# Optimization experiments

Measured on AMD Instinct MI355X. Metric: run time of the kernel, lower is better.

## Reference

```python
import jax, jax.numpy as jnp
import numpy as np

NC = 1      # constants.nc (Game-of-Life grid channels)
GRID = 32
PAD_ITERS = 31


def _iterated_wrap_idx(n, p):
    # Faithfully simulate p iterations of circular pad-1 on a growing axis.
    # NOTE: this is NOT a single wrap-pad of p; the border alternates 0/n-1.
    idx = np.arange(n)
    for _ in range(p):
        idx = np.concatenate([idx[-1:], idx, idx[:1]])
    return jnp.asarray(idx)

_IDX = _iterated_wrap_idx(GRID, PAD_ITERS)  # length 94, static


def _pad(x):
    # one gather per spatial dim replaces the 31-iteration concat loop
    return x[:, :, _IDX][:, :, :, _IDX]


def _conv(x, w, b, stride):
    y = jax.lax.conv_general_dilated(
        x, w, window_strides=(stride, stride), padding='VALID',
        dimension_numbers=('NCHW', 'OIHW', 'NCHW'))
    return y + b[None, :, None, None]


def setup_inputs() -> dict:
    key = jax.random.key(0)
    ks = jax.random.split(key, 7)
    B = 16
    s_in = 1.0 / np.sqrt(NC * 32 * 32)      # fan-in init, keeps activations sane
    s_hid = 1.0 / np.sqrt(32 * 32 * 32)
    s_out = 1.0 / np.sqrt(32)
    return {
        'x': jax.random.normal(ks[0], (B, NC, GRID, GRID), jnp.float32),
        'in_w': jax.random.normal(ks[1], (32, NC, 32, 32), jnp.float32) * s_in,
        'in_b': jnp.zeros((32,), jnp.float32),
        'convs_w': jax.random.normal(ks[2], (20, 32, 32, 32, 32), jnp.float32) * s_hid,
        'convs_b': jnp.zeros((20, 32), jnp.float32),
        'out_w': jax.random.normal(ks[3], (NC, 32, 1, 1), jnp.float32) * s_out,
        'out_b': jnp.zeros((NC,), jnp.float32),
    }


def reference(x, in_w, in_b, convs_w, convs_b, out_w, out_b):
    # in_conv: pad(31 iters) + conv k=32 s=2 (no ReLU, as in original)
    h = _conv(_pad(x), in_w, in_b, 2)           # [B,32,32,32]

    def step(h, wb):
        w, b = wb
        h = jax.nn.relu(_conv(_pad(h), w, b, 2))
        return h, None

    h, _ = jax.lax.scan(step, h, (convs_w, convs_b))  # 20 hidden layers
    return _conv(h, out_w, out_b, 1)             # 1x1 out conv, no activation
```

## Files before the change

### kernel.cpp

```cpp
#include <hip/hip_runtime.h>


typedef _Float16 f16;
typedef _Float16 f16x8 __attribute__((ext_vector_type(8)));
typedef float f32x4 __attribute__((ext_vector_type(4)));
typedef float f32x16 __attribute__((ext_vector_type(16)));
typedef int i32x4 __attribute__((ext_vector_type(4)));

__device__ __forceinline__ int mwrap(int j) {
  int t = j - 31;
  if ((unsigned)t <= 31u) return t;
  if (t < 0) return (j & 1) ? 0 : 31;
  return (j & 1) ? 0 : 31;
}


#define GLD16(dst, off, base, imm)                                          \
  asm volatile("global_load_dwordx4 %0, %1, %2 offset:%3"                   \
               : "=v"(dst) : "v"(off), "s"(base), "i"(imm) : "memory")

#define PINN(N)                                                             \
  asm volatile("s_waitcnt vmcnt(" #N ")" ::: "memory");                     \
  __builtin_amdgcn_sched_barrier(0)

#define MFMAC(AUSE, FD)                                                      \
  {                                                                          \
    __builtin_amdgcn_s_setprio(1);                                           \
    _Pragma("unroll")                                                        \
    for (int kyi_ = 0; kyi_ < 4; ++kyi_) {                                   \
      _Pragma("unroll")                                                      \
      for (int kxh_ = 0; kxh_ < 2; ++kxh_) {                                 \
        const f16x8 a_ = __builtin_bit_cast(f16x8, AUSE[kyi_ * 2 + kxh_]);   \
        acc0 = __builtin_amdgcn_mfma_f32_32x32x16_f16(a_, FD[kyi_][kxh_],    \
                                                      acc0, 0, 0, 0);        \
        acc1 = __builtin_amdgcn_mfma_f32_32x32x16_f16(a_, FD[kyi_ + 2][kxh_],\
                                                      acc1, 0, 0, 0);        \
      }                                                                      \
    }                                                                        \
    __builtin_amdgcn_s_setprio(0);                                           \
  }

template <int CIN, bool RELU, bool PRE>
__global__ __launch_bounds__(512, 2) void gemm3(
    const void* __restrict__ Wv,
    const f16* __restrict__ hp_in,
    const float* __restrict__ bias,
    f16* __restrict__ hp_out) {
  __shared__ float Red[8][2][1024];
  __shared__ __align__(16) f16 Stage[8][2][576];

  const int tid = threadIdx.x;
  const int lane = tid & 63;
  const int w = tid >> 6;
  const int ox = lane & 31;
  const int s = lane >> 5;

  const int pair0 = blockIdx.x * 2;
  const int b = pair0 >> 5;
  const int oy0 = pair0 & 31;

  const int r0 = lane / 12, g0 = lane - r0 * 12;
  const int y0 = mwrap(2 * oy0 + 4 * w + r0);
  const int y5 = mwrap(2 * oy0 + 4 * w + 5);
  int* SW = (int*)&Stage[w][0][0];
  const int wo0 = r0 * 48 + g0 * 4;
  const int wo1 = 5 * 48 + (4 + lane) * 4;
  const int bi = ox + 4 * s;

  f32x16 acc0 = {}, acc1 = {};
  i32x4 A0[8], A1[8];
  f16x8 F[6][2];
  i32x4 saA = {}, sbA = {}, saB = {}, sbB = {};

  const f16* Wl = (const f16*)Wv;
  const f16* hpb = hp_in + (size_t)b * CIN * 3072;
  const uint32_t aBase = (uint32_t)(w * 8192 + lane * 16);
  const uint32_t s0Base = (uint32_t)(y0 * 192 + g0 * 16);
  const uint32_t s1Base = (uint32_t)(y5 * 192 + 64 + (lane & 7) * 16);

  auto loadAasm = [&](int c, i32x4* dst) {
    const uint32_t o0 = aBase + (uint32_t)c * 65536u;
    const uint32_t o1 = o0 + 4096u;
    GLD16(dst[0], o0, Wl, 0);    GLD16(dst[1], o0, Wl, 1024);
    GLD16(dst[2], o0, Wl, 2048); GLD16(dst[3], o0, Wl, 3072);
    GLD16(dst[4], o1, Wl, 0);    GLD16(dst[5], o1, Wl, 1024);
    GLD16(dst[6], o1, Wl, 2048); GLD16(dst[7], o1, Wl, 3072);
  };
  auto loadSasm = [&](int c, i32x4& a, i32x4& bq) {
    const uint32_t o0 = s0Base + (uint32_t)c * 6144u;
    const uint32_t o1 = s1Base + (uint32_t)c * 6144u;
    GLD16(a, o0, hpb, 0);
    GLD16(bq, o1, hpb, 0);
  };

  auto loadA_c = [&](int c, i32x4* dst) {
#pragma unroll
    for (int kyi = 0; kyi < 4; ++kyi) {
#pragma unroll
      for (int kxh = 0; kxh < 2; ++kxh) {
        const int ky = 4 * w + kyi;
        const int chunk = (c * 32 + ky) * 2 + kxh;
        if constexpr (PRE) {
          dst[kyi * 2 + kxh] = *(const i32x4*)(Wl + (size_t)chunk * 512 + lane * 8);
        } else {
          const float* Wf = (const float*)Wv;
          const float* sp = Wf + (((size_t)(ox * CIN + c) * 32 + ky) * 32 + kxh * 16 + s * 8);
          f32x4 u0 = *(const f32x4*)sp;
          f32x4 u1 = *(const f32x4*)(sp + 4);
          f16x8 v;
          v[0] = (f16)u0[0]; v[1] = (f16)u0[1]; v[2] = (f16)u0[2]; v[3] = (f16)u0[3];
          v[4] = (f16)u1[0]; v[5] = (f16)u1[1]; v[6] = (f16)u1[2]; v[7] = (f16)u1[3];
          dst[kyi * 2 + kxh] = __builtin_bit_cast(i32x4, v);
        }
      }
    }
  };
  auto loadS_c = [&](int c, i32x4& a, i32x4& bq) {
    const int* p = (const int*)hpb + c * 1536;
    a = *(const i32x4*)(p + (y0 * 48 + g0 * 4));
    if (lane < 8) bq = *(const i32x4*)(p + (y5 * 48 + (4 + lane) * 4));
  };
  auto writeS = [&](int slot, const i32x4& a, const i32x4& bq) {
    int* q = SW + slot * 288;
    *(i32x4*)(q + wo0) = a;
    if (lane < 8) *(i32x4*)(q + wo1) = bq;
  };
  auto gathF = [&](int slot) {
    const int* q = SW + slot * 288;
#pragma unroll
    for (int j = 0; j < 6; ++j) {
      const int* R = q + j * 48 + bi;
      i32x4 t0, t1;
      t0.x = R[0]; t0.y = R[1]; t0.z = R[2]; t0.w = R[3];
      t1.x = R[8]; t1.y = R[9]; t1.z = R[10]; t1.w = R[11];
      F[j][0] = __builtin_bit_cast(f16x8, t0);
      F[j][1] = __builtin_bit_cast(f16x8, t1);
    }
  };

  if constexpr (CIN == 1) {
    loadS_c(0, saA, sbA);
    loadA_c(0, A0);
    writeS(0, saA, sbA);
    gathF(0);
    MFMAC(A0, F);
  } else if constexpr (PRE) {
    static_assert(CIN >= 4 && CIN % 2 == 0, "CIN must be 1 or even >= 4");
    loadSasm(0, saA, sbA);
    loadSasm(1, saB, sbB);
    loadAasm(0, A0);
    PINN(10);
    writeS(0, saA, sbA);
    gathF(0);
#pragma unroll 1
    for (int c = 0; c < CIN; c += 2) {
      const int cA = c + 1 < CIN ? c + 1 : CIN - 1;
      const int cS = c + 2 < CIN ? c + 2 : CIN - 1;
      loadAasm(cA, A1);
      loadSasm(cS, saA, sbA);
      PINN(10);
      MFMAC(A0, F);
      writeS(1, saB, sbB);
      gathF(1);
      const int cA2 = c + 2 < CIN ? c + 2 : CIN - 1;
      const int cS2 = c + 3 < CIN ? c + 3 : CIN - 1;
      loadAasm(cA2, A0);
      loadSasm(cS2, saB, sbB);
      PINN(10);
      MFMAC(A1, F);
      writeS(0, saA, sbA);
      gathF(0);
    }
    PINN(0);
  } else {
    loadS_c(0, saA, sbA);
    loadS_c(1, saB, sbB);
    loadA_c(0, A0);
    writeS(0, saA, sbA);
    gathF(0);
#pragma unroll 1
    for (int c = 0; c < CIN; c += 2) {
      loadA_c(c + 1 < CIN ? c + 1 : CIN - 1, A1);
      loadS_c(c + 2 < CIN ? c + 2 : CIN - 1, saA, sbA);
      MFMAC(A0, F);
      writeS(1, saB, sbB);
      gathF(1);
      loadA_c(c + 2 < CIN ? c + 2 : CIN - 1, A0);
      loadS_c(c + 3 < CIN ? c + 3 : CIN - 1, saB, sbB);
      MFMAC(A1, F);
      writeS(0, saA, sbA);
      gathF(0);
    }
  }

  __syncthreads();
#pragma unroll
  for (int r = 0; r < 16; ++r) {
    Red[w][0][r * 64 + lane] = acc0[r];
    Red[w][1][r * 64 + lane] = acc1[r];
  }
  __syncthreads();

#pragma unroll
  for (int k4 = 0; k4 < 4; ++k4) {
    const int o = tid + 512 * k4;
    const int p = o >> 10, co = (o >> 5) & 31, oxx = o & 31;
    const int idx = ((co & 3) + 4 * (co >> 3)) * 64 + ((co >> 2) & 1) * 32 + oxx;
    float v = bias[co];
#pragma unroll
    for (int w8 = 0; w8 < 8; ++w8) v += Red[w8][p][idx];
    if (RELU) v = fmaxf(v, 0.f);
    const f16 hv = (f16)v;
    f16* base = hp_out + ((size_t)(b * 32 + co) * 32 + (oy0 + p)) * 96;
    base[oxx + 31] = hv;
    if (oxx == 0) {
#pragma unroll
      for (int j = 1; j <= 29; j += 2) base[j] = hv;
#pragma unroll
      for (int j = 63; j <= 93; j += 2) base[j] = hv;
    }
    if (oxx == 31) {
#pragma unroll
      for (int j = 0; j <= 30; j += 2) base[j] = hv;
#pragma unroll
      for (int j = 64; j <= 92; j += 2) base[j] = hv;
    }
  }
}

__global__ void pad_x_kernel(const float* __restrict__ x, f16* __restrict__ xp) {
  const int i = blockIdx.x * 256 + threadIdx.x;
  if (i >= 48128) return;
  const int bq = i / 3008, r = i - bq * 3008;
  const int y = r / 94, j = r - y * 94;
  xp[bq * 3072 + y * 96 + j] = (f16)x[(bq * 32 + y) * 32 + mwrap(j)];
}

__global__ void convert_w3(const float* __restrict__ in_w,
                           const float* __restrict__ convs_w,
                           f16* __restrict__ WfIn, f16* __restrict__ WfH) {
  const int total = 4096 + 20 * 131072;
  for (int g = blockIdx.x * blockDim.x + threadIdx.x; g < total;
       g += gridDim.x * blockDim.x) {
    const float* src;
    f16* dst;
    int chunk, lanE, c, ky, kxh;
    if (g < 4096) {
      chunk = g >> 6; lanE = g & 63;
      kxh = chunk & 1; ky = chunk >> 1; c = 0;
      const int co = lanE & 31, ss = lanE >> 5;
      src = in_w + ((size_t)(co * 1 + 0) * 32 + ky) * 32 + kxh * 16 + ss * 8;
      dst = WfIn + (size_t)chunk * 512 + lanE * 8;
    } else {
      const int h = g - 4096;
      const int layer = h >> 17, r = h & 131071;
      chunk = r >> 6; lanE = r & 63;
      kxh = chunk & 1;
      const int t = chunk >> 1;
      ky = t & 31; c = t >> 5;
      const int co = lanE & 31, ss = lanE >> 5;
      src = convs_w + (size_t)layer * 1048576 +
            ((size_t)(co * 32 + c) * 32 + ky) * 32 + kxh * 16 + ss * 8;
      dst = WfH + (size_t)layer * 1048576 + (size_t)chunk * 512 + lanE * 8;
    }
    f32x4 u0 = *(const f32x4*)src;
    f32x4 u1 = *(const f32x4*)(src + 4);
    f16x8 v;
    v[0] = (f16)u0[0]; v[1] = (f16)u0[1]; v[2] = (f16)u0[2]; v[3] = (f16)u0[3];
    v[4] = (f16)u1[0]; v[5] = (f16)u1[1]; v[6] = (f16)u1[2]; v[7] = (f16)u1[3];
    *(f16x8*)dst = v;
  }
}

__global__ void out_conv3(const f16* __restrict__ hp,
                          const float* __restrict__ ow,
                          const float* __restrict__ ob,
                          float* __restrict__ out) {
  const int o = blockIdx.x * 256 + threadIdx.x;
  const int b = o >> 10, oy = (o >> 5) & 31, oxx = o & 31;
  float s = ob[0];
#pragma unroll
  for (int c = 0; c < 32; ++c)
    s += ow[c] * (float)hp[((size_t)(b * 32 + c) * 32 + oy) * 96 + oxx + 31];
  out[o] = s;
}

extern "C" void kernel_launch(void* const* d_in, const int* in_sizes, int n_in,
                              void* d_out, int out_size, void* d_ws,
                              size_t ws_size, hipStream_t stream) {
  const float* x = (const float*)d_in[0];
  const float* in_w = (const float*)d_in[1];
  const float* in_b = (const float*)d_in[2];
  const float* convs_w = (const float*)d_in[3];
  const float* convs_b = (const float*)d_in[4];
  const float* out_w = (const float*)d_in[5];
  const float* out_b = (const float*)d_in[6];
  float* out = (float*)d_out;

  char* ws = (char*)d_ws;
  f16* xpad = (f16*)ws;
  f16* hpA = (f16*)(ws + 98304);
  f16* hpB = (f16*)(ws + 98304 + 3145728);
  f16* WfIn = (f16*)(ws + 6389760);
  f16* WfH = (f16*)(ws + 6455296);
  const bool pre = (ws_size >= 48398336ull);

  pad_x_kernel<<<188, 256, 0, stream>>>(x, xpad);
  if (pre) convert_w3<<<2048, 256, 0, stream>>>(in_w, convs_w, WfIn, WfH);

  if (pre)
    gemm3<1, false, true><<<256, 512, 0, stream>>>(WfIn, xpad, in_b, hpA);
  else
    gemm3<1, false, false><<<256, 512, 0, stream>>>(in_w, xpad, in_b, hpA);

  for (int l = 0; l < 20; ++l) {
    const f16* cur = (l % 2 == 0) ? hpA : hpB;
    f16* nxt = (l % 2 == 0) ? hpB : hpA;
    if (pre)
      gemm3<32, true, true><<<256, 512, 0, stream>>>(
          WfH + (size_t)l * 1048576, cur, convs_b + 32 * l, nxt);
    else
      gemm3<32, true, false><<<256, 512, 0, stream>>>(
          convs_w + (size_t)l * 1048576, cur, convs_b + 32 * l, nxt);
  }

  out_conv3<<<64, 256, 0, stream>>>(hpA, out_w, out_b, out);
}
```

Measured before the change: 864.9 us.

## Double-buffer B fragments and deepen LDS staging ring to overlap gather with MFMA

The PRE path now keeps two register sets of B fragments (F0/F1) and a four-slot LDS staging ring, so the shared-memory write and fragment gather for the next channel are issued before the MFMAs of the current one. Stage loads run one channel further ahead. The aim is to hide LDS latency behind MFMA work instead of serialising MFMA then gather. In exchange it uses more registers and LDS, which may reduce occupancy under the launch bounds of 512 threads and 2 blocks.

```diff
diff --git a/kernel.cpp b/kernel.cpp
--- a/kernel.cpp
+++ b/kernel.cpp
@@ -22,6 +22,8 @@
 #define PINN(N)                                                             \
   asm volatile("s_waitcnt vmcnt(" #N ")" ::: "memory");                     \
   __builtin_amdgcn_sched_barrier(0)
+
+#define SBAR() __builtin_amdgcn_sched_barrier(0)
 
 #define MFMAC(AUSE, FD)                                                      \
   {                                                                          \
@@ -47,7 +49,7 @@
     const float* __restrict__ bias,
     f16* __restrict__ hp_out) {
   __shared__ float Red[8][2][1024];
-  __shared__ __align__(16) f16 Stage[8][2][576];
+  __shared__ __align__(16) f16 Stage[8][4][576];
 
   const int tid = threadIdx.x;
   const int lane = tid & 63;
@@ -69,7 +71,7 @@
 
   f32x16 acc0 = {}, acc1 = {};
   i32x4 A0[8], A1[8];
-  f16x8 F[6][2];
+  f16x8 F0[6][2], F1[6][2];
   i32x4 saA = {}, sbA = {}, saB = {}, sbB = {};
 
   const f16* Wl = (const f16*)Wv;
@@ -125,7 +127,7 @@
     *(i32x4*)(q + wo0) = a;
     if (lane < 8) *(i32x4*)(q + wo1) = bq;
   };
-  auto gathF = [&](int slot) {
+  auto gathF = [&](int slot, f16x8 (*FD)[2]) {
     const int* q = SW + slot * 288;
 #pragma unroll
     for (int j = 0; j < 6; ++j) {
@@ -133,8 +135,8 @@
       i32x4 t0, t1;
       t0.x = R[0]; t0.y = R[1]; t0.z = R[2]; t0.w = R[3];
       t1.x = R[8]; t1.y = R[9]; t1.z = R[10]; t1.w = R[11];
-      F[j][0] = __builtin_bit_cast(f16x8, t0);
-      F[j][1] = __builtin_bit_cast(f16x8, t1);
+      FD[j][0] = __builtin_bit_cast(f16x8, t0);
+      FD[j][1] = __builtin_bit_cast(f16x8, t1);
     }
   };
 
@@ -142,34 +144,35 @@
     loadS_c(0, saA, sbA);
     loadA_c(0, A0);
     writeS(0, saA, sbA);
-    gathF(0);
-    MFMAC(A0, F);
+    gathF(0, F0);
+    MFMAC(A0, F0);
   } else if constexpr (PRE) {
-    static_assert(CIN >= 4 && CIN % 2 == 0, "CIN must be 1 or even >= 4");
+    static_assert(CIN >= 6 && CIN % 2 == 0, "CIN must be 1 or even >= 6");
     loadSasm(0, saA, sbA);
     loadSasm(1, saB, sbB);
     loadAasm(0, A0);
     PINN(10);
     writeS(0, saA, sbA);
-    gathF(0);
+    loadSasm(2, saA, sbA);
+    PINN(10);
+    writeS(1, saB, sbB);
+    gathF(0, F0);
 #pragma unroll 1
     for (int c = 0; c < CIN; c += 2) {
-      const int cA = c + 1 < CIN ? c + 1 : CIN - 1;
-      const int cS = c + 2 < CIN ? c + 2 : CIN - 1;
-      loadAasm(cA, A1);
-      loadSasm(cS, saA, sbA);
+      loadAasm(c + 1 < CIN ? c + 1 : CIN - 1, A1);
+      loadSasm(c + 3 < CIN ? c + 3 : CIN - 1, saB, sbB);
       PINN(10);
-      MFMAC(A0, F);
-      writeS(1, saB, sbB);
-      gathF(1);
-      const int cA2 = c + 2 < CIN ? c + 2 : CIN - 1;
-      const int cS2 = c + 3 < CIN ? c + 3 : CIN - 1;
-      loadAasm(cA2, A0);
-      loadSasm(cS2, saB, sbB);
+      writeS((c + 2) & 3, saA, sbA);
+      gathF((c + 1) & 3, F1);
+      SBAR();
+      MFMAC(A0, F0);
+      loadAasm(c + 2 < CIN ? c + 2 : CIN - 1, A0);
+      loadSasm(c + 4 < CIN ? c + 4 : CIN - 1, saA, sbA);
       PINN(10);
-      MFMAC(A1, F);
-      writeS(0, saA, sbA);
-      gathF(0);
+      writeS((c + 3) & 3, saB, sbB);
+      gathF((c + 2) & 3, F0);
+      SBAR();
+      MFMAC(A1, F1);
     }
     PINN(0);
   } else {
@@ -177,19 +180,19 @@
     loadS_c(1, saB, sbB);
     loadA_c(0, A0);
     writeS(0, saA, sbA);
-    gathF(0);
+    gathF(0, F0);
 #pragma unroll 1
     for (int c = 0; c < CIN; c += 2) {
       loadA_c(c + 1 < CIN ? c + 1 : CIN - 1, A1);
       loadS_c(c + 2 < CIN ? c + 2 : CIN - 1, saA, sbA);
-      MFMAC(A0, F);
+      MFMAC(A0, F0);
       writeS(1, saB, sbB);
-      gathF(1);
+      gathF(1, F0);
       loadA_c(c + 2 < CIN ? c + 2 : CIN - 1, A0);
       loadS_c(c + 3 < CIN ? c + 3 : CIN - 1, saB, sbB);
-      MFMAC(A1, F);
+      MFMAC(A1, F0);
       writeS(0, saA, sbA);
-      gathF(0);
+      gathF(0, F0);
     }
   }
 
```

Result: no change. 853.4 us (-1.3%).
